# Kernel tuning notes

Measured on AMD Instinct MI355X. Metric: run time of the kernel, lower is better.

## Reference

```python
import jax, jax.numpy as jnp
import numpy as np

B, C, H = 16, 256, 32          # batch, in_channels(=out_channels), image_size
HEADS, HS = 8, 32              # heads = out_channels // head_size
D = HEADS * HS                 # head_dim = 256
N = H * H                      # tokens = 1024
EPS = 1e-5


def _rel_indices(h, w):
    # Faithful port of RelativeAttention2d.get_indices
    y = np.arange(h)
    x = np.arange(w)
    y1, x1, y2, x2 = np.meshgrid(y, x, y, x, indexing='ij')
    idx = (y1 - y2 + h - 1) * (2 * w - 1) + (x1 - x2 + w - 1)
    return jnp.asarray(idx.reshape(-1), dtype=jnp.int32)  # [N*N]


def setup_inputs() -> dict:
    key = jax.random.key(0)
    ks = jax.random.split(key, 10)
    s = 0.02
    return {
        'x': jax.random.normal(ks[0], (B, C, H, H), jnp.float32),
        'ln_g': jnp.ones((C,), jnp.float32),
        'ln_b': jnp.zeros((C,), jnp.float32),
        'wq': jax.random.normal(ks[1], (D, C), jnp.float32) * s,
        'bq': jnp.zeros((D,), jnp.float32),
        'wk': jax.random.normal(ks[2], (D, C), jnp.float32) * s,
        'bk': jnp.zeros((D,), jnp.float32),
        'wv': jax.random.normal(ks[3], (D, C), jnp.float32) * s,
        'bv': jnp.zeros((D,), jnp.float32),
        'wo': jax.random.normal(ks[4], (C, D), jnp.float32) * s,
        'bo': jnp.zeros((C,), jnp.float32),
        'rel_bias': jax.random.normal(ks[5], (HEADS, (2 * H - 1) * (2 * H - 1)), jnp.float32),
        'rel_idx': _rel_indices(H, H),
    }


def reference(x, ln_g, ln_b, wq, bq, wk, bk, wv, bv, wo, bo, rel_bias, rel_idx):
    b = x.shape[0]
    # norm(): LayerNorm over channel axis (dim 1 after the double transpose)
    mu = jnp.mean(x, axis=1, keepdims=True)
    var = jnp.mean((x - mu) ** 2, axis=1, keepdims=True)
    xn = (x - mu) / jnp.sqrt(var + EPS)
    xn = xn * ln_g[None, :, None, None] + ln_b[None, :, None, None]
    # reshape_for_linear: raw reshape [b, C, H, W] -> [b, N, C] (as in torch)
    xr = xn.reshape(b, N, C)
    # projections, then raw view(b, heads, head_size, -1) as in torch
    q = (xr @ wq.T + bq).reshape(b, HEADS, HS, N)
    k = (xr @ wk.T + bk).reshape(b, HEADS, HS, N)
    v = (xr @ wv.T + bv).reshape(b, HEADS, HS, N)
    # dots = k^T q / sqrt(head_dim)   [b, heads, N, N]
    dots = jnp.einsum('bhdn,bhdm->bhnm', k, q) / np.float32(np.sqrt(D))
    # gathered relative position bias  [heads, N, N]
    bias = rel_bias[:, rel_idx].reshape(HEADS, N, N)
    attn = jax.nn.softmax(dots + bias[None], axis=-2)  # non-standard softmax dim
    # out = v @ attn  [b, heads, head_size, N]
    out = jnp.einsum('bhdn,bhnm->bhdm', v, attn)
    out = out.reshape(b, H, H, D)  # raw view as in torch
    out = out @ wo.T + bo          # to_output linear (dropout is identity in eval)
    out = out.reshape(b, C, H, H)  # raw view back to [b, out_channels, H, W]
    return x + out
```

## Files before the change

kernel.cpp:

```cpp
#include <hip/hip_runtime.h>
#include <cstdint>

#define PERB 262144
#define LOG2EF 1.4426950408889634f
#define C1F 0.09016844005556022f

typedef __attribute__((ext_vector_type(8))) short bf16x8;
typedef __attribute__((ext_vector_type(4))) float f32x4;
typedef unsigned short ushort_t;

__device__ __forceinline__ uint16_t f2bf(float f) {
    uint32_t u = __float_as_uint(f);
    u += 0x7fff + ((u >> 16) & 1);
    return (uint16_t)(u >> 16);
}

__device__ __forceinline__ void glds16(const void* g, void* l) {
    __builtin_amdgcn_global_load_lds(
        (const __attribute__((address_space(1))) void*)g,
        (__attribute__((address_space(3))) void*)l, 16, 0, 0);
}

__global__ __launch_bounds__(256) void prep_kernel(
    const float* __restrict__ x, const float* __restrict__ gam,
    const float* __restrict__ bet, ushort_t* __restrict__ X,
    const float* __restrict__ wq, const float* __restrict__ wk,
    const float* __restrict__ wv, const float* __restrict__ wo,
    ushort_t* __restrict__ oq, ushort_t* __restrict__ ok,
    ushort_t* __restrict__ ov, ushort_t* __restrict__ oo,
    const float* __restrict__ rb, float* __restrict__ rb2)
{
    const int blk = blockIdx.x;
    const int tid = threadIdx.x;
    if (blk < 256) {
        const int which = blk >> 6;
        const int idx = ((blk & 63) * 256 + tid) * 4;
        const float* src = which == 0 ? wq : which == 1 ? wk : which == 2 ? wv : wo;
        ushort_t* dst    = which == 0 ? oq : which == 1 ? ok : which == 2 ? ov : oo;
        const float4 v = *(const float4*)&src[idx];
        uint2 p;
        p.x = (uint32_t)f2bf(v.x) | ((uint32_t)f2bf(v.y) << 16);
        p.y = (uint32_t)f2bf(v.z) | ((uint32_t)f2bf(v.w) << 16);
        *(uint2*)&dst[idx] = p;
        return;
    }
    if (blk >= 512) {
        const int h = blk - 512;
        const float* s = rb + h * 3969;
        float* d = rb2 + h * 3969;
        for (int i = tid; i < 3969; i += 256) d[i] = s[i] * LOG2EF;
        return;
    }
    const int lb  = blk - 256;
    const int b   = lb >> 4;
    const int sp0 = (lb & 15) << 6;
    const int v   = tid & 15;
    const int cg  = tid >> 4;
    const int sp  = sp0 + v * 4;
    const float* xb = x + (size_t)b * PERB + sp;

    float4 vals[16];
    float4 s4 = {0.f, 0.f, 0.f, 0.f}, q4 = {0.f, 0.f, 0.f, 0.f};
#pragma unroll
    for (int i = 0; i < 16; ++i) {
        const float4 t = *(const float4*)&xb[(size_t)(cg * 16 + i) * 1024];
        vals[i] = t;
        s4.x += t.x; s4.y += t.y; s4.z += t.z; s4.w += t.w;
        q4.x += t.x * t.x; q4.y += t.y * t.y; q4.z += t.z * t.z; q4.w += t.w * t.w;
    }
    __shared__ float red[2][16][64];
    __shared__ float mr[2][64];
    *(float4*)&red[0][cg][v * 4] = s4;
    *(float4*)&red[1][cg][v * 4] = q4;
    __syncthreads();
    if (tid < 64) {
        float ts = 0.f, tq = 0.f;
#pragma unroll
        for (int g = 0; g < 16; ++g) { ts += red[0][g][tid]; tq += red[1][g][tid]; }
        const float mean = ts * (1.f / 256.f);
        const float var  = tq * (1.f / 256.f) - mean * mean;
        mr[0][tid] = mean;
        mr[1][tid] = rsqrtf(var + 1e-5f);
    }
    __syncthreads();
    const float4 mean4 = *(const float4*)&mr[0][v * 4];
    const float4 rstd4 = *(const float4*)&mr[1][v * 4];

    ushort_t* Xb = X + (size_t)b * PERB + sp;
#pragma unroll
    for (int i = 0; i < 16; ++i) {
        const int c = cg * 16 + i;
        const float g = gam[c], be = bet[c];
        const float4 t = vals[i];
        const float y0 = (t.x - mean4.x) * rstd4.x * g + be;
        const float y1 = (t.y - mean4.y) * rstd4.y * g + be;
        const float y2 = (t.z - mean4.z) * rstd4.z * g + be;
        const float y3 = (t.w - mean4.w) * rstd4.w * g + be;
        uint2 p;
        p.x = (uint32_t)f2bf(y0) | ((uint32_t)f2bf(y1) << 16);
        p.y = (uint32_t)f2bf(y2) | ((uint32_t)f2bf(y3) << 16);
        *(uint2*)&Xb[(size_t)c * 1024] = p;
    }
}

__device__ __forceinline__ void qkv_stage(
    ushort_t* Sb, const ushort_t* __restrict__ X,
    const ushort_t* __restrict__ wq, const ushort_t* __restrict__ wk,
    const ushort_t* __restrict__ wv,
    int m0, int n0, int k0, int w, int lane)
{
    const int rsub = lane >> 3;
    const int u    = lane & 7;
    const int koct = u ^ rsub;
#pragma unroll
    for (int i = 0; i < 2; ++i) {
        const int rg  = w * 2 + i;
        const int row = rg * 8 + rsub;
        const int go  = k0 + koct * 8;
        ushort_t* db = Sb + rg * 512;
        glds16(&X [(size_t)(m0 + row) * 256 + go], db);
        glds16(&wq[(size_t)(n0 + row) * 256 + go], db + 4096);
        glds16(&wk[(size_t)(n0 + row) * 256 + go], db + 8192);
        glds16(&wv[(size_t)(n0 + row) * 256 + go], db + 12288);
    }
}

__device__ __forceinline__ void qkv_compute(
    const ushort_t* Sb, int w, int c, int quad, f32x4 acc[3][4])
{
#pragma unroll
    for (int ks = 0; ks < 2; ++ks) {
        const int kq = ks * 4 + quad;
        const int uo = (kq ^ (c & 7)) * 8;
        bf16x8 af[4];
#pragma unroll
        for (int msub = 0; msub < 4; ++msub)
            af[msub] = *(const bf16x8*)&Sb[(msub * 16 + c) * 64 + uo];
        bf16x8 bw[3];
#pragma unroll
        for (int o3 = 0; o3 < 3; ++o3)
            bw[o3] = *(const bf16x8*)&Sb[(o3 + 1) * 4096 + (w * 16 + c) * 64 + uo];
#pragma unroll
        for (int o3 = 0; o3 < 3; ++o3)
#pragma unroll
            for (int msub = 0; msub < 4; ++msub)
                acc[o3][msub] = __builtin_amdgcn_mfma_f32_16x16x32_bf16(
                    bw[o3], af[msub], acc[o3][msub], 0, 0, 0);
    }
}

__global__ __launch_bounds__(256) void qkv_kernel(
    const ushort_t* __restrict__ X,
    const ushort_t* __restrict__ wq, const float* __restrict__ bq,
    const ushort_t* __restrict__ wk, const float* __restrict__ bk,
    const ushort_t* __restrict__ wv, const float* __restrict__ bv,
    ushort_t* __restrict__ Q, ushort_t* __restrict__ K, ushort_t* __restrict__ V)
{
    __shared__ __align__(16) ushort_t SB0[4][4096];
    __shared__ __align__(16) ushort_t SB1[4][4096];

    const int blk = blockIdx.x;
    const int m0  = (blk >> 2) << 6;
    const int n0  = (blk & 3) << 6;
    const int tid = threadIdx.x;
    const int w    = tid >> 6;
    const int lane = tid & 63;
    const int quad = lane >> 4;
    const int c    = lane & 15;

    f32x4 acc[3][4];
#pragma unroll
    for (int o3 = 0; o3 < 3; ++o3)
#pragma unroll
        for (int i = 0; i < 4; ++i) acc[o3][i] = (f32x4){0.f, 0.f, 0.f, 0.f};

    qkv_stage(&SB0[0][0], X, wq, wk, wv, m0, n0, 0, w, lane);
    __syncthreads();
#pragma unroll
    for (int kc = 0; kc < 4; ++kc) {
        if (kc < 3) {
            if ((kc & 1) == 0)
                qkv_stage(&SB1[0][0], X, wq, wk, wv, m0, n0, (kc + 1) << 6, w, lane);
            else
                qkv_stage(&SB0[0][0], X, wq, wk, wv, m0, n0, (kc + 1) << 6, w, lane);
        }
        if ((kc & 1) == 0) qkv_compute(&SB0[0][0], w, c, quad, acc);
        else               qkv_compute(&SB1[0][0], w, c, quad, acc);
        __syncthreads();
    }

    const int n = n0 + w * 16 + quad * 4;
    const float4 bq4 = *(const float4*)&bq[n];
    const float4 bk4 = *(const float4*)&bk[n];
    const float4 bv4 = *(const float4*)&bv[n];
    ushort_t* outs[3] = {Q, K, V};
    const float4 bias[3] = {bq4, bk4, bv4};
#pragma unroll
    for (int msub = 0; msub < 4; ++msub) {
        const size_t m = (size_t)(m0 + msub * 16 + c);
#pragma unroll
        for (int o3 = 0; o3 < 3; ++o3) {
            const f32x4 a = acc[o3][msub];
            uint2 p;
            p.x = (uint32_t)f2bf(a[0] + bias[o3].x) | ((uint32_t)f2bf(a[1] + bias[o3].y) << 16);
            p.y = (uint32_t)f2bf(a[2] + bias[o3].z) | ((uint32_t)f2bf(a[3] + bias[o3].w) << 16);
            *(uint2*)&outs[o3][m * 256 + n] = p;
        }
    }
}

__global__ __launch_bounds__(256, 4) void attn_kernel(
    const ushort_t* __restrict__ Q, const ushort_t* __restrict__ K,
    const ushort_t* __restrict__ V, const float* __restrict__ relb2,
    ushort_t* __restrict__ O)
{
    __shared__ __align__(16) unsigned char smem[28672];
    char* Pb = (char*)smem;
    char* Kl = (char*)(smem + 16384);
    char* Vl = (char*)(smem + 20480);

    const int blk = blockIdx.x;
    const int bh  = blk & 127;
    const int mt  = blk >> 7;
    const int b   = bh >> 3;
    const int h   = bh & 7;
    const int m0  = mt << 7;
    const int tid = threadIdx.x;
    const int w    = tid >> 6;
    const int lane = tid & 63;
    const int quad = lane >> 4;
    const int c    = lane & 15;

    const size_t base = (size_t)b * PERB + (size_t)h * 32768;
    const ushort_t* Qg = Q + base;
    const ushort_t* Kg = K + base;
    const ushort_t* Vg = V + base;
    const float* rbh = relb2 + h * 3969;

    {
        const int mm = tid & 127;
        const int sg = tid >> 7;
        union { bf16x8 v; uint16_t u[8]; } g0, g1;
#pragma unroll
        for (int j = 0; j < 8; ++j)
            g0.u[j] = Qg[(size_t)(sg * 16 + j) * 1024 + m0 + mm];
#pragma unroll
        for (int j = 0; j < 8; ++j)
            g1.u[j] = Qg[(size_t)(sg * 16 + 8 + j) * 1024 + m0 + mm];
        *(bf16x8*)(Pb + (sg * 2 + 0) * 2048 + mm * 16) = g0.v;
        *(bf16x8*)(Pb + (sg * 2 + 1) * 2048 + mm * 16) = g1.v;
    }
    __syncthreads();
    bf16x8 qfrag[8];
#pragma unroll
    for (int msub = 0; msub < 8; ++msub)
        qfrag[msub] = *(const bf16x8*)(Pb + quad * 2048 + (msub * 16 + c) * 16);

    int moff[8];
#pragma unroll
    for (int msub = 0; msub < 8; ++msub) {
        const int m = m0 + msub * 16 + c;
        moff[msub] = 1984 - (m >> 5) * 63 - (m & 31);
    }

    f32x4 oacc[2][2], dacc[2];
#pragma unroll
    for (int i = 0; i < 2; ++i) {
        dacc[i] = (f32x4){0.f, 0.f, 0.f, 0.f};
#pragma unroll
        for (int j = 0; j < 2; ++j) oacc[i][j] = (f32x4){0.f, 0.f, 0.f, 0.f};
    }
    bf16x8 onesf;
#pragma unroll
    for (int j = 0; j < 8; ++j) onesf[j] = (short)0x3F80;

    const int knn = tid & 63, ksg = tid >> 6;
    const int vs  = tid >> 3, vng = tid & 7;
    const int kWr = ksg * 1024 + knn * 16;
    const int vWr = vs * 128 + ((vng ^ (vs & 7)) << 4);
    const int kRd = quad * 1024 + (w * 16 + c) * 16;
    const int pWr = c * 128 + (((2 * w + (quad >> 1)) ^ (c & 7)) << 4) + ((quad & 1) << 3);
    const int c7  = c & 7;

    uint32_t kpre[8]; bf16x8 vpre;
#pragma unroll
    for (int j = 0; j < 8; ++j) kpre[j] = Kg[(size_t)(ksg * 8 + j) * 1024 + knn];
    vpre = *(const bf16x8*)&Vg[(size_t)vs * 1024 + vng * 8];

    for (int ch = 0; ch < 16; ++ch) {
        const int n0c = ch << 6;
        const int cb  = ch & 1;

        {
            uint4 kp;
            kp.x = kpre[0] | (kpre[1] << 16);
            kp.y = kpre[2] | (kpre[3] << 16);
            kp.z = kpre[4] | (kpre[5] << 16);
            kp.w = kpre[6] | (kpre[7] << 16);
            *(uint4*)(Kl + kWr) = kp;
            *(bf16x8*)(Vl + cb * 4096 + vWr) = vpre;
        }
        __syncthreads();

        {
            const int n0n = ((ch + 1) & 15) << 6;
#pragma unroll
            for (int j = 0; j < 8; ++j)
                kpre[j] = Kg[(size_t)(ksg * 8 + j) * 1024 + n0n + knn];
            vpre = *(const bf16x8*)&Vg[(size_t)vs * 1024 + n0n + vng * 8];
        }

        const bf16x8 kf = *(const bf16x8*)(Kl + kRd);
        f32x4 sacc[8];
#pragma unroll
        for (int msub = 0; msub < 8; ++msub) {
            const f32x4 z = {0.f, 0.f, 0.f, 0.f};
            sacc[msub] = __builtin_amdgcn_mfma_f32_16x16x32_bf16(kf, qfrag[msub], z, 0, 0, 0);
        }

        const int nbase = n0c + w * 16 + quad * 4;
        const int nidx0 = (nbase >> 5) * 63 + (nbase & 31);
#pragma unroll
        for (int msub = 0; msub < 8; ++msub) {
            const float* bp = rbh + nidx0 + moff[msub];
            float p[4];
#pragma unroll
            for (int r = 0; r < 4; ++r)
                p[r] = __builtin_amdgcn_exp2f(fmaf(sacc[msub][r], C1F, bp[r]));
            uint2 pk;
            pk.x = __builtin_amdgcn_perm(__float_as_uint(p[1]), __float_as_uint(p[0]), 0x07060302u);
            pk.y = __builtin_amdgcn_perm(__float_as_uint(p[3]), __float_as_uint(p[2]), 0x07060302u);
            *(uint2*)(Pb + msub * 2048 + pWr) = pk;
        }
        __syncthreads();

#pragma unroll
        for (int kstep = 0; kstep < 2; ++kstep) {
            const int u = ((kstep * 4 + quad) ^ c7) << 4;
            const bf16x8 vf0 = *(const bf16x8*)(Vl + cb * 4096 + c * 128 + u);
            const bf16x8 vf1 = *(const bf16x8*)(Vl + cb * 4096 + (16 + c) * 128 + u);
#pragma unroll
            for (int mi = 0; mi < 2; ++mi) {
                const bf16x8 pf = *(const bf16x8*)(Pb + ((w * 2 + mi) * 16 + c) * 128 + u);
                oacc[0][mi] = __builtin_amdgcn_mfma_f32_16x16x32_bf16(vf0, pf, oacc[0][mi], 0, 0, 0);
                oacc[1][mi] = __builtin_amdgcn_mfma_f32_16x16x32_bf16(vf1, pf, oacc[1][mi], 0, 0, 0);
                dacc[mi]    = __builtin_amdgcn_mfma_f32_16x16x32_bf16(onesf, pf, dacc[mi], 0, 0, 0);
            }
        }
    }

    ushort_t* Ob = O + base;
#pragma unroll
    for (int mi = 0; mi < 2; ++mi) {
        const float inv = 1.0f / dacc[mi][0];
        const int m = m0 + (w * 2 + mi) * 16 + c;
#pragma unroll
        for (int ssub = 0; ssub < 2; ++ssub)
#pragma unroll
            for (int r = 0; r < 4; ++r)
                Ob[(size_t)(ssub * 16 + quad * 4 + r) * 1024 + m] = f2bf(oacc[ssub][mi][r] * inv);
    }
}

__device__ __forceinline__ void oproj_stage(
    ushort_t* Sb, const ushort_t* __restrict__ A, const ushort_t* __restrict__ wo,
    int m0, int n0, int k0, int w, int lane)
{
    const int rsub = lane >> 3;
    const int u    = lane & 7;
    const int koct = u ^ rsub;
#pragma unroll
    for (int i = 0; i < 2; ++i) {
        const int rg  = w * 2 + i;
        const int row = rg * 8 + rsub;
        const int go  = k0 + koct * 8;
        ushort_t* db = Sb + rg * 512;
        glds16(&A [(size_t)(m0 + row) * 256 + go], db);
        glds16(&wo[(size_t)(n0 + row) * 256 + go], db + 4096);
    }
}

__device__ __forceinline__ void oproj_compute(
    const ushort_t* Sb, int w, int c, int quad, f32x4 acc[4])
{
#pragma unroll
    for (int ks = 0; ks < 2; ++ks) {
        const int kq = ks * 4 + quad;
        const int uo = (kq ^ (c & 7)) * 8;
        const bf16x8 bw = *(const bf16x8*)&Sb[4096 + (w * 16 + c) * 64 + uo];
#pragma unroll
        for (int msub = 0; msub < 4; ++msub) {
            const bf16x8 af = *(const bf16x8*)&Sb[(msub * 16 + c) * 64 + uo];
            acc[msub] = __builtin_amdgcn_mfma_f32_16x16x32_bf16(bw, af, acc[msub], 0, 0, 0);
        }
    }
}

__global__ __launch_bounds__(256, 4) void oproj_kernel(
    const ushort_t* __restrict__ A, const ushort_t* __restrict__ wo,
    const float* __restrict__ bo, const float* __restrict__ x,
    float* __restrict__ out)
{
    __shared__ __align__(16) ushort_t SA0[2][4096];
    __shared__ __align__(16) ushort_t SA1[2][4096];

    const int blk = blockIdx.x;
    const int m0  = (blk >> 2) << 6;
    const int n0  = (blk & 3) << 6;
    const int tid = threadIdx.x;
    const int w    = tid >> 6;
    const int lane = tid & 63;
    const int quad = lane >> 4;
    const int c    = lane & 15;

    f32x4 acc[4];
#pragma unroll
    for (int i = 0; i < 4; ++i) acc[i] = (f32x4){0.f, 0.f, 0.f, 0.f};

    oproj_stage(&SA0[0][0], A, wo, m0, n0, 0, w, lane);
    __syncthreads();
#pragma unroll
    for (int kc = 0; kc < 4; ++kc) {
        if (kc < 3) {
            if ((kc & 1) == 0)
                oproj_stage(&SA1[0][0], A, wo, m0, n0, (kc + 1) << 6, w, lane);
            else
                oproj_stage(&SA0[0][0], A, wo, m0, n0, (kc + 1) << 6, w, lane);
        }
        if ((kc & 1) == 0) oproj_compute(&SA0[0][0], w, c, quad, acc);
        else               oproj_compute(&SA1[0][0], w, c, quad, acc);
        __syncthreads();
    }

    const int n = n0 + w * 16 + quad * 4;
    const float4 bo4 = *(const float4*)&bo[n];
#pragma unroll
    for (int msub = 0; msub < 4; ++msub) {
        const size_t g = (size_t)(m0 + msub * 16 + c) * 256 + n;
        const float4 r = *(const float4*)&x[g];
        float4 t;
        t.x = acc[msub][0] + bo4.x + r.x;
        t.y = acc[msub][1] + bo4.y + r.y;
        t.z = acc[msub][2] + bo4.z + r.z;
        t.w = acc[msub][3] + bo4.w + r.w;
        *(float4*)&out[g] = t;
    }
}

extern "C" void kernel_launch(void* const* d_in, const int* in_sizes, int n_in,
                              void* d_out, int out_size, void* d_ws, size_t ws_size,
                              hipStream_t stream)
{
    (void)in_sizes; (void)n_in; (void)out_size; (void)ws_size;
    const float* x   = (const float*)d_in[0];
    const float* lng = (const float*)d_in[1];
    const float* lnb = (const float*)d_in[2];
    const float* wq  = (const float*)d_in[3];
    const float* bq  = (const float*)d_in[4];
    const float* wk  = (const float*)d_in[5];
    const float* bk  = (const float*)d_in[6];
    const float* wv  = (const float*)d_in[7];
    const float* bv  = (const float*)d_in[8];
    const float* wo  = (const float*)d_in[9];
    const float* bo  = (const float*)d_in[10];
    const float* rb  = (const float*)d_in[11];

    ushort_t* ws = (ushort_t*)d_ws;
    ushort_t* Xbf = ws;
    ushort_t* Qbf = ws + 1 * 4194304;
    ushort_t* Kbf = ws + 2 * 4194304;
    ushort_t* Vbf = ws + 3 * 4194304;
    ushort_t* Obf = ws + 4 * 4194304;
    ushort_t* Wqb = ws + 5 * 4194304;
    ushort_t* Wkb = Wqb + 65536;
    ushort_t* Wvb = Wkb + 65536;
    ushort_t* Wob = Wvb + 65536;
    float* rb2 = (float*)(Wob + 65536);
    float* out = (float*)d_out;

    hipLaunchKernelGGL(prep_kernel,  dim3(520),  dim3(256), 0, stream,
                       x, lng, lnb, Xbf, wq, wk, wv, wo, Wqb, Wkb, Wvb, Wob, rb, rb2);
    hipLaunchKernelGGL(qkv_kernel,   dim3(1024), dim3(256), 0, stream,
                       Xbf, Wqb, bq, Wkb, bk, Wvb, bv, Qbf, Kbf, Vbf);
    hipLaunchKernelGGL(attn_kernel,  dim3(1024), dim3(256), 0, stream, Qbf, Kbf, Vbf, rb2, Obf);
    hipLaunchKernelGGL(oproj_kernel, dim3(1024), dim3(256), 0, stream, Obf, Wob, bo, x, out);
}
```

Measured before the change: 161.7 us.

## Give each wave its own query rows in attention to drop per-chunk barrier

```diff
diff --git a/kernel.cpp b/kernel.cpp
--- a/kernel.cpp
+++ b/kernel.cpp
@@ -214,10 +214,10 @@
     const ushort_t* __restrict__ V, const float* __restrict__ relb2,
     ushort_t* __restrict__ O)
 {
-    __shared__ __align__(16) unsigned char smem[28672];
+    __shared__ __align__(16) unsigned char smem[32768];
     char* Pb = (char*)smem;
     char* Kl = (char*)(smem + 16384);
-    char* Vl = (char*)(smem + 20480);
+    char* Vl = (char*)(smem + 24576);
 
     const int blk = blockIdx.x;
     const int bh  = blk & 127;
@@ -237,6 +237,17 @@
     const ushort_t* Vg = V + base;
     const float* rbh = relb2 + h * 3969;
 
+    const int knn = tid & 63, ksg = tid >> 6;
+    const int vs  = tid >> 3, vng = tid & 7;
+    const int kWr = ksg * 1024 + knn * 16;
+    const int vWr = vs * 128 + ((vng ^ (vs & 7)) << 4);
+    const int c7  = c & 7;
+
+    uint32_t kpre[8]; bf16x8 vpre;
+#pragma unroll
+    for (int j = 0; j < 8; ++j) kpre[j] = Kg[(size_t)(ksg * 8 + j) * 1024 + knn];
+    vpre = *(const bf16x8*)&Vg[(size_t)vs * 1024 + vng * 8];
+
     {
         const int mm = tid & 127;
         const int sg = tid >> 7;
@@ -250,18 +261,31 @@
         *(bf16x8*)(Pb + (sg * 2 + 0) * 2048 + mm * 16) = g0.v;
         *(bf16x8*)(Pb + (sg * 2 + 1) * 2048 + mm * 16) = g1.v;
     }
+    {
+        uint4 kp;
+        kp.x = kpre[0] | (kpre[1] << 16);
+        kp.y = kpre[2] | (kpre[3] << 16);
+        kp.z = kpre[4] | (kpre[5] << 16);
+        kp.w = kpre[6] | (kpre[7] << 16);
+        *(uint4*)(Kl + kWr) = kp;
+        *(bf16x8*)(Vl + vWr) = vpre;
+    }
     __syncthreads();
-    bf16x8 qfrag[8];
-#pragma unroll
-    for (int msub = 0; msub < 8; ++msub)
-        qfrag[msub] = *(const bf16x8*)(Pb + quad * 2048 + (msub * 16 + c) * 16);
-
-    int moff[8];
-#pragma unroll
-    for (int msub = 0; msub < 8; ++msub) {
-        const int m = m0 + msub * 16 + c;
-        moff[msub] = 1984 - (m >> 5) * 63 - (m & 31);
-    }
+
+    bf16x8 qfrag[2];
+#pragma unroll
+    for (int mi = 0; mi < 2; ++mi)
+        qfrag[mi] = *(const bf16x8*)(Pb + quad * 2048 + (((w * 2 + mi) * 16 + c)) * 16);
+    __syncthreads();
+
+    int moff[2];
+#pragma unroll
+    for (int mi = 0; mi < 2; ++mi) {
+        const int m = m0 + (w * 2 + mi) * 16 + c;
+        moff[mi] = 1984 - (m >> 5) * 63 - (m & 31);
+    }
+    const int rowb0 = ((w * 2 + 0) * 16 + c) * 128;
+    const int rowb1 = ((w * 2 + 1) * 16 + c) * 128;
 
     f32x4 oacc[2][2], dacc[2];
 #pragma unroll
@@ -274,79 +298,82 @@
 #pragma unroll
     for (int j = 0; j < 8; ++j) onesf[j] = (short)0x3F80;
 
-    const int knn = tid & 63, ksg = tid >> 6;
-    const int vs  = tid >> 3, vng = tid & 7;
-    const int kWr = ksg * 1024 + knn * 16;
-    const int vWr = vs * 128 + ((vng ^ (vs & 7)) << 4);
-    const int kRd = quad * 1024 + (w * 16 + c) * 16;
-    const int pWr = c * 128 + (((2 * w + (quad >> 1)) ^ (c & 7)) << 4) + ((quad & 1) << 3);
-    const int c7  = c & 7;
-
-    uint32_t kpre[8]; bf16x8 vpre;
-#pragma unroll
-    for (int j = 0; j < 8; ++j) kpre[j] = Kg[(size_t)(ksg * 8 + j) * 1024 + knn];
-    vpre = *(const bf16x8*)&Vg[(size_t)vs * 1024 + vng * 8];
+#pragma unroll
+    for (int j = 0; j < 8; ++j) kpre[j] = Kg[(size_t)(ksg * 8 + j) * 1024 + 64 + knn];
+    vpre = *(const bf16x8*)&Vg[(size_t)vs * 1024 + 64 + vng * 8];
 
     for (int ch = 0; ch < 16; ++ch) {
         const int n0c = ch << 6;
         const int cb  = ch & 1;
-
-        {
+        const char* Kc = Kl + (cb << 12);
+        const char* Vc = Vl + (cb << 12);
+
+        bf16x8 kf[4];
+#pragma unroll
+        for (int nsub = 0; nsub < 4; ++nsub)
+            kf[nsub] = *(const bf16x8*)(Kc + quad * 1024 + (nsub * 16 + c) * 16);
+        f32x4 sacc[2][4];
+#pragma unroll
+        for (int mi = 0; mi < 2; ++mi)
+#pragma unroll
+            for (int nsub = 0; nsub < 4; ++nsub) {
+                const f32x4 z = {0.f, 0.f, 0.f, 0.f};
+                sacc[mi][nsub] = __builtin_amdgcn_mfma_f32_16x16x32_bf16(
+                    kf[nsub], qfrag[mi], z, 0, 0, 0);
+            }
+
+#pragma unroll
+        for (int mi = 0; mi < 2; ++mi) {
+            const int rowb = mi ? rowb1 : rowb0;
+#pragma unroll
+            for (int nsub = 0; nsub < 4; ++nsub) {
+                const int nbase = n0c + nsub * 16 + quad * 4;
+                const int nidx0 = (nbase >> 5) * 63 + (nbase & 31);
+                const float* bp = rbh + nidx0 + moff[mi];
+                float p[4];
+#pragma unroll
+                for (int r = 0; r < 4; ++r)
+                    p[r] = __builtin_amdgcn_exp2f(fmaf(sacc[mi][nsub][r], C1F, bp[r]));
+                uint2 pk;
+                pk.x = __builtin_amdgcn_perm(__float_as_uint(p[1]), __float_as_uint(p[0]), 0x07060302u);
+                pk.y = __builtin_amdgcn_perm(__float_as_uint(p[3]), __float_as_uint(p[2]), 0x07060302u);
+                const int u = (2 * nsub + (quad >> 1)) ^ c7;
+                *(uint2*)(Pb + rowb + u * 16 + ((quad & 1) << 3)) = pk;
+            }
+        }
+
+#pragma unroll
+        for (int kstep = 0; kstep < 2; ++kstep) {
+            const int u = ((kstep * 4 + quad) ^ c7) << 4;
+            const bf16x8 vf0 = *(const bf16x8*)(Vc + c * 128 + u);
+            const bf16x8 vf1 = *(const bf16x8*)(Vc + (16 + c) * 128 + u);
+#pragma unroll
+            for (int mi = 0; mi < 2; ++mi) {
+                const bf16x8 pf = *(const bf16x8*)(Pb + (mi ? rowb1 : rowb0) + u);
+                oacc[0][mi] = __builtin_amdgcn_mfma_f32_16x16x32_bf16(vf0, pf, oacc[0][mi], 0, 0, 0);
+                oacc[1][mi] = __builtin_amdgcn_mfma_f32_16x16x32_bf16(vf1, pf, oacc[1][mi], 0, 0, 0);
+                dacc[mi]    = __builtin_amdgcn_mfma_f32_16x16x32_bf16(onesf, pf, dacc[mi], 0, 0, 0);
+            }
+        }
+
+        if (ch < 15) {
+            const int nb = (cb ^ 1) << 12;
             uint4 kp;
             kp.x = kpre[0] | (kpre[1] << 16);
             kp.y = kpre[2] | (kpre[3] << 16);
             kp.z = kpre[4] | (kpre[5] << 16);
             kp.w = kpre[6] | (kpre[7] << 16);
-            *(uint4*)(Kl + kWr) = kp;
-            *(bf16x8*)(Vl + cb * 4096 + vWr) = vpre;
+            *(uint4*)(Kl + nb + kWr) = kp;
+            *(bf16x8*)(Vl + nb + vWr) = vpre;
+            if (ch < 14) {
+                const int n0n = (ch + 2) << 6;
+#pragma unroll
+                for (int j = 0; j < 8; ++j)
+                    kpre[j] = Kg[(size_t)(ksg * 8 + j) * 1024 + n0n + knn];
+                vpre = *(const bf16x8*)&Vg[(size_t)vs * 1024 + n0n + vng * 8];
+            }
         }
         __syncthreads();
-
-        {
-            const int n0n = ((ch + 1) & 15) << 6;
-#pragma unroll
-            for (int j = 0; j < 8; ++j)
-                kpre[j] = Kg[(size_t)(ksg * 8 + j) * 1024 + n0n + knn];
-            vpre = *(const bf16x8*)&Vg[(size_t)vs * 1024 + n0n + vng * 8];
-        }
-
-        const bf16x8 kf = *(const bf16x8*)(Kl + kRd);
-        f32x4 sacc[8];
-#pragma unroll
-        for (int msub = 0; msub < 8; ++msub) {
-            const f32x4 z = {0.f, 0.f, 0.f, 0.f};
-            sacc[msub] = __builtin_amdgcn_mfma_f32_16x16x32_bf16(kf, qfrag[msub], z, 0, 0, 0);
-        }
-
-        const int nbase = n0c + w * 16 + quad * 4;
-        const int nidx0 = (nbase >> 5) * 63 + (nbase & 31);
-#pragma unroll
-        for (int msub = 0; msub < 8; ++msub) {
-            const float* bp = rbh + nidx0 + moff[msub];
-            float p[4];
-#pragma unroll
-            for (int r = 0; r < 4; ++r)
-                p[r] = __builtin_amdgcn_exp2f(fmaf(sacc[msub][r], C1F, bp[r]));
-            uint2 pk;
-            pk.x = __builtin_amdgcn_perm(__float_as_uint(p[1]), __float_as_uint(p[0]), 0x07060302u);
-            pk.y = __builtin_amdgcn_perm(__float_as_uint(p[3]), __float_as_uint(p[2]), 0x07060302u);
-            *(uint2*)(Pb + msub * 2048 + pWr) = pk;
-        }
-        __syncthreads();
-
-#pragma unroll
-        for (int kstep = 0; kstep < 2; ++kstep) {
-            const int u = ((kstep * 4 + quad) ^ c7) << 4;
-            const bf16x8 vf0 = *(const bf16x8*)(Vl + cb * 4096 + c * 128 + u);
-            const bf16x8 vf1 = *(const bf16x8*)(Vl + cb * 4096 + (16 + c) * 128 + u);
-#pragma unroll
-            for (int mi = 0; mi < 2; ++mi) {
-                const bf16x8 pf = *(const bf16x8*)(Pb + ((w * 2 + mi) * 16 + c) * 128 + u);
-                oacc[0][mi] = __builtin_amdgcn_mfma_f32_16x16x32_bf16(vf0, pf, oacc[0][mi], 0, 0, 0);
-                oacc[1][mi] = __builtin_amdgcn_mfma_f32_16x16x32_bf16(vf1, pf, oacc[1][mi], 0, 0, 0);
-                dacc[mi]    = __builtin_amdgcn_mfma_f32_16x16x32_bf16(onesf, pf, dacc[mi], 0, 0, 0);
-            }
-        }
     }
 
     ushort_t* Ob = O + base;
```

After: 156.6 us (median of 2 runs). -3.2%, faster.
